# Kernel tuning notes

Hardware: AMD Instinct MI355X
Metric: run time of the kernel (lower is better)

Reference implementation:

```python
import jax, jax.numpy as jnp
import numpy as np

HEADS = 16
DIM_HEAD = 64


def setup_inputs() -> dict:
    key = jax.random.key(0)
    k1, k2, k3, k4 = jax.random.split(key, 4)
    b, sq, skv, dim = 2, 2048, 2048, 1024
    inner = HEADS * DIM_HEAD
    return {
        "x_q": jax.random.normal(k1, (b, sq, dim), dtype=jnp.float32),
        "x_kv": jax.random.normal(k2, (b, skv, dim), dtype=jnp.float32),
        "W_qkv": jax.random.normal(k3, (dim, 3 * inner), dtype=jnp.float32) * (dim ** -0.5),
        "W_out": jax.random.normal(k4, (inner, dim), dtype=jnp.float32) * (inner ** -0.5),
        "b_out": jnp.zeros((dim,), dtype=jnp.float32),
    }


def reference(x_q, x_kv, W_qkv, W_out, b_out):
    b, sq, dim = x_q.shape
    skv = x_kv.shape[1]
    inner = HEADS * DIM_HEAD
    scale = DIM_HEAD ** -0.5
    # to_qkv on concat([x_q, x_kv], seq) as in the original (bias-free linear)
    qkv = jnp.concatenate([x_q, x_kv], axis=1) @ W_qkv  # [b, sq+skv, 3*inner]
    q, k, v = jnp.split(qkv, 3, axis=-1)
    q = q[:, :sq].reshape(b, sq, HEADS, DIM_HEAD).transpose(0, 2, 1, 3)   # [b,h,sq,d]
    k = k[:, sq:].reshape(b, skv, HEADS, DIM_HEAD).transpose(0, 2, 1, 3)  # [b,h,skv,d]
    v = v[:, sq:].reshape(b, skv, HEADS, DIM_HEAD).transpose(0, 2, 1, 3)  # [b,h,skv,d]
    dots = jnp.einsum('bhqd,bhkd->bhqk', q, k) * scale
    attn = jax.nn.softmax(dots, axis=-1)  # dropout p=0.0 -> identity
    out = jnp.einsum('bhqk,bhkd->bhqd', attn, v)
    out = out.transpose(0, 2, 1, 3).reshape(b, sq, inner)
    return out @ W_out + b_out
```

## Files before the change

kernel.cpp:

```cpp
#include <hip/hip_runtime.h>


typedef __attribute__((ext_vector_type(8))) short short8;
typedef __attribute__((ext_vector_type(4))) short short4v;
typedef __attribute__((ext_vector_type(4))) float floatx4;

#define QSCALE 0.18033688f

#if __has_builtin(__builtin_amdgcn_exp2f)
#define EXP2(x) __builtin_amdgcn_exp2f(x)
#else
#define EXP2(x) exp2f(x)
#endif

__device__ __forceinline__ ushort f2b(float f) {
  union { float f; unsigned u; } x; x.f = f;
  unsigned r = (x.u + 0x7fffu + ((x.u >> 16) & 1u)) >> 16;
  return (ushort)r;
}

__device__ __forceinline__ unsigned f2b2(float a, float b) {
  union { float f; unsigned u; } x, y; x.f = a; y.f = b;
  return __builtin_amdgcn_perm(y.u + 0x8000u, x.u + 0x8000u, 0x07060302u);
}

#define GLL(gp, lp)                                                            \
  __builtin_amdgcn_global_load_lds(                                            \
      (const __attribute__((address_space(1))) void*)(gp),                     \
      (__attribute__((address_space(3))) void*)(lp), 16, 0, 0)

__global__ void cvt2(const float* __restrict__ a, const float* __restrict__ bsrc,
                     ushort* __restrict__ oa, ushort* __restrict__ ob, int n) {
  int half = gridDim.x >> 1;
  bool lo = (int)blockIdx.x < half;
  const float* in = lo ? a : bsrc;
  ushort* out = lo ? oa : ob;
  int bid = lo ? blockIdx.x : blockIdx.x - half;
  int stride = half * blockDim.x * 4;
  for (int i = (bid * blockDim.x + threadIdx.x) * 4; i < n; i += stride) {
    float4 v = *(const float4*)(in + i);
    uint2 o;
    o.x = f2b2(v.x, v.y);
    o.y = f2b2(v.z, v.w);
    *(uint2*)(out + i) = o;
  }
}

__global__ void transposeW(const float* __restrict__ Wqkv, ushort* __restrict__ WqkvT,
                           const float* __restrict__ Wout, ushort* __restrict__ WoutT) {
  __shared__ float tile[32][33];
  bool first = blockIdx.x < 96;
  const float* in = first ? Wqkv : Wout;
  ushort* out = first ? WqkvT : WoutT;
  int N = first ? 3072 : 1024;
  int bx = first ? blockIdx.x : blockIdx.x - 96;
  int k0 = blockIdx.y * 32, n0 = bx * 32;
  int tx = threadIdx.x, ty = threadIdx.y;
#pragma unroll
  for (int i = 0; i < 32; i += 8)
    tile[ty + i][tx] = in[(size_t)(k0 + ty + i) * N + n0 + tx];
  __syncthreads();
#pragma unroll
  for (int i = 0; i < 32; i += 8)
    out[(size_t)(n0 + ty + i) * 1024 + k0 + tx] = f2b(tile[tx][ty + i]);
}

__global__ __launch_bounds__(256, 3) void gemm_qkv(
    const ushort* __restrict__ Aq, const ushort* __restrict__ Akv,
    const ushort* __restrict__ Bt,
    ushort* __restrict__ Cq, ushort* __restrict__ Ck, ushort* __restrict__ Cv) {
  __shared__ __align__(16) ushort As[2][128 * 32];
  __shared__ __align__(16) ushort Bs[2][128 * 32];
  const int n0 = blockIdx.x * 128, m0 = blockIdx.y * 128;
  const ushort* A = (blockIdx.x >= 8) ? Akv : Aq;
  const int t = threadIdx.x;
  const int w = t >> 6, lane = t & 63, dl = lane & 15, g = lane >> 4;
  const int wm = (w >> 1) * 64, wn = (w & 1) * 64;
  const int K = 1024;

  auto stage = [&](int buf, int k0) {
#pragma unroll
    for (int p = 0; p < 2; p++) {
      int j = t + p * 256;
      int row = j >> 2, slot = j & 3, c = (slot - row) & 3;
      GLL(A + (size_t)(m0 + row) * K + k0 + c * 8, &As[buf][j * 8]);
    }
#pragma unroll
    for (int p = 0; p < 2; p++) {
      int j = t + p * 256;
      int row = j >> 2, slot = j & 3, c = (slot - row) & 3;
      GLL(Bt + (size_t)(n0 + row) * K + k0 + c * 8, &Bs[buf][j * 8]);
    }
  };

  const floatx4 fz = {0.f, 0.f, 0.f, 0.f};
  floatx4 acc[4][4];
#pragma unroll
  for (int i = 0; i < 4; i++)
#pragma unroll
    for (int j = 0; j < 4; j++) acc[i][j] = fz;

  stage(0, 0);
  for (int kt = 0; kt < 32; kt++) {
    int cur = kt & 1;
    __builtin_amdgcn_s_waitcnt(0);
    __syncthreads();
    if (kt + 1 < 32) stage(cur ^ 1, (kt + 1) * 32);
    short8 af[4], bf[4];
#pragma unroll
    for (int mt = 0; mt < 4; mt++) {
      int row = wm + mt * 16 + dl;
      af[mt] = *(const short8*)&As[cur][row * 32 + ((g + row) & 3) * 8];
    }
#pragma unroll
    for (int nt = 0; nt < 4; nt++) {
      int row = wn + nt * 16 + dl;
      bf[nt] = *(const short8*)&Bs[cur][row * 32 + ((g + row) & 3) * 8];
    }
#pragma unroll
    for (int mt = 0; mt < 4; mt++)
#pragma unroll
      for (int nt = 0; nt < 4; nt++)
        acc[mt][nt] = __builtin_amdgcn_mfma_f32_16x16x32_bf16(af[mt], bf[nt], acc[mt][nt], 0, 0, 0);
  }

#pragma unroll
  for (int mt = 0; mt < 4; mt++)
#pragma unroll
    for (int nt = 0; nt < 4; nt++) {
      int gcol = n0 + wn + nt * 16 + dl;
      int row0 = m0 + wm + mt * 16 + g * 4;
      if (gcol < 1024) {
#pragma unroll
        for (int r = 0; r < 4; r++)
          Cq[(size_t)(row0 + r) * 1024 + gcol] = f2b(acc[mt][nt][r] * QSCALE);
      } else if (gcol < 2048) {
#pragma unroll
        for (int r = 0; r < 4; r++)
          Ck[(size_t)(row0 + r) * 1024 + gcol - 1024] = f2b(acc[mt][nt][r]);
      } else {
        uint2 pk;
        pk.x = f2b2(acc[mt][nt][0], acc[mt][nt][1]);
        pk.y = f2b2(acc[mt][nt][2], acc[mt][nt][3]);
        *(uint2*)(Cv + ((size_t)(row0 >> 11) * 1024 + (gcol - 2048)) * 2048 +
                  (row0 & 2047)) = pk;
      }
    }
}

__global__ __launch_bounds__(256, 3) void gemm_out(
    const ushort* __restrict__ A, const ushort* __restrict__ Bt,
    float* __restrict__ C, const float* __restrict__ bias) {
  __shared__ __align__(16) ushort As[2][128 * 64];
  __shared__ __align__(16) ushort Bs[2][64 * 64];
  const int n0 = blockIdx.x * 64, m0 = blockIdx.y * 128;
  const int t = threadIdx.x;
  const int w = t >> 6, lane = t & 63, dl = lane & 15, g = lane >> 4;
  const int wm = (w >> 1) * 64, wn = (w & 1) * 32;
  const int K = 1024;

  auto stage = [&](int buf, int k0) {
#pragma unroll
    for (int p = 0; p < 4; p++) {
      int j = t + p * 256;
      int row = j >> 3, slot = j & 7, c = (slot - row) & 7;
      GLL(A + (size_t)(m0 + row) * K + k0 + c * 8, &As[buf][j * 8]);
    }
#pragma unroll
    for (int p = 0; p < 2; p++) {
      int j = t + p * 256;
      int row = j >> 3, slot = j & 7, c = (slot - row) & 7;
      GLL(Bt + (size_t)(n0 + row) * K + k0 + c * 8, &Bs[buf][j * 8]);
    }
  };

  const floatx4 fz = {0.f, 0.f, 0.f, 0.f};
  floatx4 acc[4][2];
#pragma unroll
  for (int i = 0; i < 4; i++)
#pragma unroll
    for (int j = 0; j < 2; j++) acc[i][j] = fz;

  stage(0, 0);
  for (int kt = 0; kt < 16; kt++) {
    int cur = kt & 1;
    __builtin_amdgcn_s_waitcnt(0);
    __syncthreads();
    if (kt + 1 < 16) stage(cur ^ 1, (kt + 1) * 64);
#pragma unroll
    for (int ks = 0; ks < 2; ks++) {
      short8 af[4], bf[2];
#pragma unroll
      for (int mt = 0; mt < 4; mt++) {
        int row = wm + mt * 16 + dl;
        af[mt] = *(const short8*)&As[cur][row * 64 + ((ks * 4 + g + row) & 7) * 8];
      }
#pragma unroll
      for (int nt = 0; nt < 2; nt++) {
        int row = wn + nt * 16 + dl;
        bf[nt] = *(const short8*)&Bs[cur][row * 64 + ((ks * 4 + g + row) & 7) * 8];
      }
#pragma unroll
      for (int mt = 0; mt < 4; mt++)
#pragma unroll
        for (int nt = 0; nt < 2; nt++)
          acc[mt][nt] = __builtin_amdgcn_mfma_f32_16x16x32_bf16(af[mt], bf[nt], acc[mt][nt], 0, 0, 0);
    }
  }
#pragma unroll
  for (int mt = 0; mt < 4; mt++)
#pragma unroll
    for (int nt = 0; nt < 2; nt++) {
      int gcol = n0 + wn + nt * 16 + dl;
      int row0 = m0 + wm + mt * 16 + g * 4;
      float badd = bias[gcol];
#pragma unroll
      for (int r = 0; r < 4; r++)
        C[(size_t)(row0 + r) * 1024 + gcol] = acc[mt][nt][r] + badd;
    }
}

__global__ __launch_bounds__(256, 2) void attn(
    const ushort* __restrict__ Qb,
    const ushort* __restrict__ Kb,
    const ushort* __restrict__ Vt,
    ushort* __restrict__ Ob) {
  __shared__ __align__(16) ushort Ks[2][64 * 64];
  __shared__ __align__(16) ushort Vs[2][64 * 64];
  __shared__ __align__(16) ushort Pq[128 * 64];

  const int bh = blockIdx.x, b = bh >> 4, h = bh & 15;
  const int q0 = blockIdx.y * 128;
  const int t = threadIdx.x, w = t >> 6, lane = t & 63, dl = lane & 15, g = lane >> 4;

  const ushort* Kg = Kb + (size_t)(b * 2048) * 1024 + h * 64;
  const ushort* Vg = Vt + (size_t)(b * 1024 + h * 64) * 2048;

  short8 bq[2][2];
#pragma unroll
  for (int nt = 0; nt < 2; nt++) {
    int qa = q0 + w * 32 + nt * 16 + dl;
    const ushort* qrow = Qb + (size_t)(b * 2048 + qa) * 1024 + h * 64;
    bq[nt][0] = *(const short8*)(qrow + g * 8);
    bq[nt][1] = *(const short8*)(qrow + 32 + g * 8);
  }

  auto stageK = [&](int buf, int kv0) {
#pragma unroll
    for (int p = 0; p < 2; p++) {
      int j = t + p * 256;
      int row = j >> 3, slot = j & 7, c = (slot - row) & 7;
      GLL(Kg + (size_t)(kv0 + row) * 1024 + c * 8, &Ks[buf][j * 8]);
    }
  };
  auto stageV = [&](int buf, int kv0) {
#pragma unroll
    for (int p = 0; p < 2; p++) {
      int j = t + p * 256;
      int row = j >> 3, slot = j & 7, c = (slot - row) & 7;
      GLL(Vg + (size_t)row * 2048 + kv0 + c * 8, &Vs[buf][j * 8]);
    }
  };
  stageK(0, 0);
  stageV(0, 0);

  const floatx4 fz = {0.f, 0.f, 0.f, 0.f};
  floatx4 o[4][2];
#pragma unroll
  for (int i = 0; i < 4; i++)
#pragma unroll
    for (int n = 0; n < 2; n++) o[i][n] = fz;
  floatx4 l4[2] = {fz, fz};

  for (int it = 0; it < 32; it++) {
    int cur = it & 1;
    __builtin_amdgcn_s_waitcnt(0);
    __syncthreads();
    if (it + 1 < 32) { stageK(cur ^ 1, (it + 1) * 64); stageV(cur ^ 1, (it + 1) * 64); }

    floatx4 s[4][2];
#pragma unroll
    for (int mt = 0; mt < 4; mt++)
#pragma unroll
      for (int nt = 0; nt < 2; nt++) s[mt][nt] = fz;
#pragma unroll
    for (int ks = 0; ks < 2; ks++) {
      short8 a[4];
#pragma unroll
      for (int mt = 0; mt < 4; mt++) {
        int row = mt * 16 + dl;
        a[mt] = *(const short8*)&Ks[cur][row * 64 + ((ks * 4 + g + row) & 7) * 8];
      }
#pragma unroll
      for (int mt = 0; mt < 4; mt++)
#pragma unroll
        for (int nt = 0; nt < 2; nt++)
          s[mt][nt] = __builtin_amdgcn_mfma_f32_16x16x32_bf16(a[mt], bq[nt][ks], s[mt][nt], 0, 0, 0);
    }

#pragma unroll
    for (int nt = 0; nt < 2; nt++)
#pragma unroll
      for (int mt = 0; mt < 4; mt++) {
#pragma unroll
        for (int r = 0; r < 4; r++) s[mt][nt][r] = EXP2(s[mt][nt][r]);
        l4[nt] += s[mt][nt];
      }

#pragma unroll
    for (int nt = 0; nt < 2; nt++) {
      int qr = w * 32 + nt * 16 + dl;
#pragma unroll
      for (int mt = 0; mt < 4; mt++) {
        uint2 pk;
        pk.x = f2b2(s[mt][nt][0], s[mt][nt][1]);
        pk.y = f2b2(s[mt][nt][2], s[mt][nt][3]);
        *(uint2*)&Pq[qr * 64 + ((mt * 4 + g + qr) & 15) * 4] = pk;
      }
    }
    asm volatile("" ::: "memory");

#pragma unroll
    for (int ks2 = 0; ks2 < 2; ks2++) {
      short8 av[4], bp[2];
#pragma unroll
      for (int mtd = 0; mtd < 4; mtd++) {
        int row = mtd * 16 + dl;
        av[mtd] = *(const short8*)&Vs[cur][row * 64 + ((ks2 * 4 + g + row) & 7) * 8];
      }
#pragma unroll
      for (int nt = 0; nt < 2; nt++) {
        int qr = w * 32 + nt * 16 + dl;
        int sq = ks2 * 8 + 2 * g;
        short4v lo = *(const short4v*)&Pq[qr * 64 + ((sq + qr) & 15) * 4];
        short4v hi = *(const short4v*)&Pq[qr * 64 + ((sq + 1 + qr) & 15) * 4];
        bp[nt] = short8{lo.x, lo.y, lo.z, lo.w, hi.x, hi.y, hi.z, hi.w};
      }
#pragma unroll
      for (int mtd = 0; mtd < 4; mtd++)
#pragma unroll
        for (int nt = 0; nt < 2; nt++)
          o[mtd][nt] = __builtin_amdgcn_mfma_f32_16x16x32_bf16(av[mtd], bp[nt], o[mtd][nt], 0, 0, 0);
    }
    asm volatile("" ::: "memory");
  }

  float inv_l[2];
#pragma unroll
  for (int nt = 0; nt < 2; nt++) {
    float l = (l4[nt][0] + l4[nt][1]) + (l4[nt][2] + l4[nt][3]);
    l += __shfl_xor(l, 16);
    l += __shfl_xor(l, 32);
    inv_l[nt] = 1.f / l;
  }

#pragma unroll
  for (int nt = 0; nt < 2; nt++) {
    int qr = w * 32 + nt * 16 + dl;
#pragma unroll
    for (int mtd = 0; mtd < 4; mtd++) {
      uint2 pk;
      pk.x = f2b2(o[mtd][nt][0] * inv_l[nt], o[mtd][nt][1] * inv_l[nt]);
      pk.y = f2b2(o[mtd][nt][2] * inv_l[nt], o[mtd][nt][3] * inv_l[nt]);
      *(uint2*)&Pq[qr * 64 + ((mtd * 4 + g + qr) & 15) * 4] = pk;
    }
  }
  asm volatile("" ::: "memory");
#pragma unroll
  for (int p = 0; p < 4; p++) {
    int j = lane + p * 64;
    int r32 = j >> 3, c = j & 7;
    int qr = w * 32 + r32;
    short4v lo = *(const short4v*)&Pq[qr * 64 + ((2 * c + qr) & 15) * 4];
    short4v hi = *(const short4v*)&Pq[qr * 64 + ((2 * c + 1 + qr) & 15) * 4];
    short8 v = {lo.x, lo.y, lo.z, lo.w, hi.x, hi.y, hi.z, hi.w};
    *(short8*)(Ob + (size_t)(b * 2048 + q0 + qr) * 1024 + h * 64 + c * 8) = v;
  }
}

extern "C" void kernel_launch(void* const* d_in, const int* in_sizes, int n_in,
                              void* d_out, int out_size, void* d_ws, size_t ws_size,
                              hipStream_t stream) {
  const float* x_q  = (const float*)d_in[0];
  const float* x_kv = (const float*)d_in[1];
  const float* Wqkv = (const float*)d_in[2];
  const float* Wout = (const float*)d_in[3];
  const float* bout = (const float*)d_in[4];
  float* out = (float*)d_out;

  char* p = (char*)d_ws;
  ushort* Xq    = (ushort*)p; p += (size_t)4096 * 1024 * 2;
  ushort* Xkv   = (ushort*)p; p += (size_t)4096 * 1024 * 2;
  ushort* WqkvT = (ushort*)p; p += (size_t)3072 * 1024 * 2;
  ushort* WoutT = (ushort*)p; p += (size_t)1024 * 1024 * 2;
  ushort* Qb    = (ushort*)p; p += (size_t)4096 * 1024 * 2;
  ushort* Kb    = (ushort*)p; p += (size_t)4096 * 1024 * 2;
  ushort* Vt    = (ushort*)p; p += (size_t)2 * 1024 * 2048 * 2;
  ushort* Ob    = (ushort*)p; p += (size_t)4096 * 1024 * 2;

  cvt2<<<2048, 256, 0, stream>>>(x_q, x_kv, Xq, Xkv, 4096 * 1024);
  transposeW<<<dim3(128, 32), dim3(32, 8), 0, stream>>>(Wqkv, WqkvT, Wout, WoutT);
  gemm_qkv<<<dim3(24, 32), 256, 0, stream>>>(Xq, Xkv, WqkvT, Qb, Kb, Vt);
  attn<<<dim3(32, 16), 256, 0, stream>>>(Qb, Kb, Vt, Ob);
  gemm_out<<<dim3(16, 32), 256, 0, stream>>>(Ob, WoutT, out, bout);
}
```

Baseline: 197.9 us.

## Split attention KV tile across wave pairs and halve query tile per block

The attention kernel now processes 64 queries per block instead of 128. Its four waves form two query groups times two KV halves, each wave covering 32 KV columns per tile. Partial outputs and row sums from the two KV halves are reduced through shared memory at the end, and the grid doubles to 1024 blocks with launch bounds raised to 4 blocks per SM. The aim is more parallelism and occupancy, at the cost of re-streaming K/V per block (twice the global K/V traffic), an extra LDS reduction, and more register pressure under the tighter launch bound.

```diff
diff --git a/kernel.cpp b/kernel.cpp
--- a/kernel.cpp
+++ b/kernel.cpp
@@ -220,18 +220,19 @@
     }
 }
 
-__global__ __launch_bounds__(256, 2) void attn(
+__global__ __launch_bounds__(256, 4) void attn(
     const ushort* __restrict__ Qb,
     const ushort* __restrict__ Kb,
     const ushort* __restrict__ Vt,
     ushort* __restrict__ Ob) {
   __shared__ __align__(16) ushort Ks[2][64 * 64];
   __shared__ __align__(16) ushort Vs[2][64 * 64];
-  __shared__ __align__(16) ushort Pq[128 * 64];
+  __shared__ __align__(16) ushort Pq[64 * 64];
 
   const int bh = blockIdx.x, b = bh >> 4, h = bh & 15;
-  const int q0 = blockIdx.y * 128;
+  const int q0 = blockIdx.y * 64;
   const int t = threadIdx.x, w = t >> 6, lane = t & 63, dl = lane & 15, g = lane >> 4;
+  const int wq = w & 1, wkv = w >> 1;
 
   const ushort* Kg = Kb + (size_t)(b * 2048) * 1024 + h * 64;
   const ushort* Vg = Vt + (size_t)(b * 1024 + h * 64) * 2048;
@@ -239,7 +240,7 @@
   short8 bq[2][2];
 #pragma unroll
   for (int nt = 0; nt < 2; nt++) {
-    int qa = q0 + w * 32 + nt * 16 + dl;
+    int qa = q0 + wq * 32 + nt * 16 + dl;
     const ushort* qrow = Qb + (size_t)(b * 2048 + qa) * 1024 + h * 64;
     bq[nt][0] = *(const short8*)(qrow + g * 8);
     bq[nt][1] = *(const short8*)(qrow + 32 + g * 8);
@@ -278,21 +279,21 @@
     __syncthreads();
     if (it + 1 < 32) { stageK(cur ^ 1, (it + 1) * 64); stageV(cur ^ 1, (it + 1) * 64); }
 
-    floatx4 s[4][2];
-#pragma unroll
-    for (int mt = 0; mt < 4; mt++)
+    floatx4 s[2][2];
+#pragma unroll
+    for (int mt = 0; mt < 2; mt++)
 #pragma unroll
       for (int nt = 0; nt < 2; nt++) s[mt][nt] = fz;
 #pragma unroll
     for (int ks = 0; ks < 2; ks++) {
-      short8 a[4];
-#pragma unroll
-      for (int mt = 0; mt < 4; mt++) {
-        int row = mt * 16 + dl;
+      short8 a[2];
+#pragma unroll
+      for (int mt = 0; mt < 2; mt++) {
+        int row = wkv * 32 + mt * 16 + dl;
         a[mt] = *(const short8*)&Ks[cur][row * 64 + ((ks * 4 + g + row) & 7) * 8];
       }
 #pragma unroll
-      for (int mt = 0; mt < 4; mt++)
+      for (int mt = 0; mt < 2; mt++)
 #pragma unroll
         for (int nt = 0; nt < 2; nt++)
           s[mt][nt] = __builtin_amdgcn_mfma_f32_16x16x32_bf16(a[mt], bq[nt][ks], s[mt][nt], 0, 0, 0);
@@ -301,7 +302,7 @@
 #pragma unroll
     for (int nt = 0; nt < 2; nt++)
 #pragma unroll
-      for (int mt = 0; mt < 4; mt++) {
+      for (int mt = 0; mt < 2; mt++) {
 #pragma unroll
         for (int r = 0; r < 4; r++) s[mt][nt][r] = EXP2(s[mt][nt][r]);
         l4[nt] += s[mt][nt];
@@ -309,72 +310,95 @@
 
 #pragma unroll
     for (int nt = 0; nt < 2; nt++) {
-      int qr = w * 32 + nt * 16 + dl;
-#pragma unroll
-      for (int mt = 0; mt < 4; mt++) {
+      int qr = wq * 32 + nt * 16 + dl;
+#pragma unroll
+      for (int mt = 0; mt < 2; mt++) {
+        int kvq = wkv * 8 + mt * 4 + g;
         uint2 pk;
         pk.x = f2b2(s[mt][nt][0], s[mt][nt][1]);
         pk.y = f2b2(s[mt][nt][2], s[mt][nt][3]);
-        *(uint2*)&Pq[qr * 64 + ((mt * 4 + g + qr) & 15) * 4] = pk;
+        *(uint2*)&Pq[qr * 64 + ((kvq + qr) & 15) * 4] = pk;
       }
     }
     asm volatile("" ::: "memory");
 
-#pragma unroll
-    for (int ks2 = 0; ks2 < 2; ks2++) {
-      short8 av[4], bp[2];
-#pragma unroll
-      for (int mtd = 0; mtd < 4; mtd++) {
-        int row = mtd * 16 + dl;
-        av[mtd] = *(const short8*)&Vs[cur][row * 64 + ((ks2 * 4 + g + row) & 7) * 8];
-      }
-#pragma unroll
-      for (int nt = 0; nt < 2; nt++) {
-        int qr = w * 32 + nt * 16 + dl;
-        int sq = ks2 * 8 + 2 * g;
-        short4v lo = *(const short4v*)&Pq[qr * 64 + ((sq + qr) & 15) * 4];
-        short4v hi = *(const short4v*)&Pq[qr * 64 + ((sq + 1 + qr) & 15) * 4];
-        bp[nt] = short8{lo.x, lo.y, lo.z, lo.w, hi.x, hi.y, hi.z, hi.w};
-      }
-#pragma unroll
-      for (int mtd = 0; mtd < 4; mtd++)
-#pragma unroll
-        for (int nt = 0; nt < 2; nt++)
-          o[mtd][nt] = __builtin_amdgcn_mfma_f32_16x16x32_bf16(av[mtd], bp[nt], o[mtd][nt], 0, 0, 0);
-    }
+    short8 av[4], bp[2];
+#pragma unroll
+    for (int mtd = 0; mtd < 4; mtd++) {
+      int row = mtd * 16 + dl;
+      av[mtd] = *(const short8*)&Vs[cur][row * 64 + ((wkv * 4 + g + row) & 7) * 8];
+    }
+#pragma unroll
+    for (int nt = 0; nt < 2; nt++) {
+      int qr = wq * 32 + nt * 16 + dl;
+      int kvq = wkv * 8 + g * 2;
+      short4v lo = *(const short4v*)&Pq[qr * 64 + ((kvq + qr) & 15) * 4];
+      short4v hi = *(const short4v*)&Pq[qr * 64 + ((kvq + 1 + qr) & 15) * 4];
+      bp[nt] = short8{lo.x, lo.y, lo.z, lo.w, hi.x, hi.y, hi.z, hi.w};
+    }
+#pragma unroll
+    for (int mtd = 0; mtd < 4; mtd++)
+#pragma unroll
+      for (int nt = 0; nt < 2; nt++)
+        o[mtd][nt] = __builtin_amdgcn_mfma_f32_16x16x32_bf16(av[mtd], bp[nt], o[mtd][nt], 0, 0, 0);
     asm volatile("" ::: "memory");
   }
 
-  float inv_l[2];
+  float lsum[2];
 #pragma unroll
   for (int nt = 0; nt < 2; nt++) {
     float l = (l4[nt][0] + l4[nt][1]) + (l4[nt][2] + l4[nt][3]);
     l += __shfl_xor(l, 16);
     l += __shfl_xor(l, 32);
-    inv_l[nt] = 1.f / l;
-  }
-
-#pragma unroll
-  for (int nt = 0; nt < 2; nt++) {
-    int qr = w * 32 + nt * 16 + dl;
-#pragma unroll
-    for (int mtd = 0; mtd < 4; mtd++) {
-      uint2 pk;
-      pk.x = f2b2(o[mtd][nt][0] * inv_l[nt], o[mtd][nt][1] * inv_l[nt]);
-      pk.y = f2b2(o[mtd][nt][2] * inv_l[nt], o[mtd][nt][3] * inv_l[nt]);
-      *(uint2*)&Pq[qr * 64 + ((mtd * 4 + g + qr) & 15) * 4] = pk;
-    }
-  }
-  asm volatile("" ::: "memory");
-#pragma unroll
-  for (int p = 0; p < 4; p++) {
-    int j = lane + p * 64;
-    int r32 = j >> 3, c = j & 7;
-    int qr = w * 32 + r32;
-    short4v lo = *(const short4v*)&Pq[qr * 64 + ((2 * c + qr) & 15) * 4];
-    short4v hi = *(const short4v*)&Pq[qr * 64 + ((2 * c + 1 + qr) & 15) * 4];
+    lsum[nt] = l;
+  }
+
+  __syncthreads();
+  float* redO = (float*)Ks;
+  float* redL = (float*)Vs;
+  if (wkv == 1) {
+#pragma unroll
+    for (int mtd = 0; mtd < 4; mtd++)
+#pragma unroll
+      for (int nt = 0; nt < 2; nt++)
+        *(floatx4*)&redO[wq * 2048 + lane * 32 + (mtd * 2 + nt) * 4] = o[mtd][nt];
+#pragma unroll
+    for (int nt = 0; nt < 2; nt++)
+      redL[wq * 32 + nt * 16 + dl] = lsum[nt];
+  }
+  __syncthreads();
+  if (wkv == 0) {
+    float inv_l[2];
+#pragma unroll
+    for (int nt = 0; nt < 2; nt++)
+      inv_l[nt] = 1.f / (lsum[nt] + redL[wq * 32 + nt * 16 + dl]);
+#pragma unroll
+    for (int mtd = 0; mtd < 4; mtd++)
+#pragma unroll
+      for (int nt = 0; nt < 2; nt++)
+        o[mtd][nt] += *(const floatx4*)&redO[wq * 2048 + lane * 32 + (mtd * 2 + nt) * 4];
+#pragma unroll
+    for (int nt = 0; nt < 2; nt++) {
+      int qr = wq * 32 + nt * 16 + dl;
+#pragma unroll
+      for (int mtd = 0; mtd < 4; mtd++) {
+        int dq = mtd * 4 + g;
+        uint2 pk;
+        pk.x = f2b2(o[mtd][nt][0] * inv_l[nt], o[mtd][nt][1] * inv_l[nt]);
+        pk.y = f2b2(o[mtd][nt][2] * inv_l[nt], o[mtd][nt][3] * inv_l[nt]);
+        *(uint2*)&Pq[qr * 64 + ((dq + qr) & 15) * 4] = pk;
+      }
+    }
+  }
+  __syncthreads();
+#pragma unroll
+  for (int p = 0; p < 2; p++) {
+    int j = t + p * 256;
+    int row = j >> 3, c = j & 7;
+    short4v lo = *(const short4v*)&Pq[row * 64 + ((2 * c + row) & 15) * 4];
+    short4v hi = *(const short4v*)&Pq[row * 64 + ((2 * c + 1 + row) & 15) * 4];
     short8 v = {lo.x, lo.y, lo.z, lo.w, hi.x, hi.y, hi.z, hi.w};
-    *(short8*)(Ob + (size_t)(b * 2048 + q0 + qr) * 1024 + h * 64 + c * 8) = v;
+    *(short8*)(Ob + (size_t)(b * 2048 + q0 + row) * 1024 + h * 64 + c * 8) = v;
   }
 }
 
@@ -401,6 +425,6 @@
   cvt2<<<2048, 256, 0, stream>>>(x_q, x_kv, Xq, Xkv, 4096 * 1024);
   transposeW<<<dim3(128, 32), dim3(32, 8), 0, stream>>>(Wqkv, WqkvT, Wout, WoutT);
   gemm_qkv<<<dim3(24, 32), 256, 0, stream>>>(Xq, Xkv, WqkvT, Qb, Kb, Vt);
-  attn<<<dim3(32, 16), 256, 0, stream>>>(Qb, Kb, Vt, Ob);
+  attn<<<dim3(32, 32), 256, 0, stream>>>(Qb, Kb, Vt, Ob);
   gemm_out<<<dim3(16, 32), 256, 0, stream>>>(Ob, WoutT, out, bout);
 }
```

Result: slower. 203.4 us (+2.8%).

## Merge prep kernels and stage V-transpose epilogue through LDS for coalesced stores

Applied to the files above, without the earlier changes.

Merges the input conversion and weight-transpose kernels into one launch to remove a kernel launch and the gap between them. In the QKV GEMM, the V-tile epilogue now writes the transposed tile into shared memory (padded stride 136) and then emits 16-byte coalesced stores to the transposed V buffer, replacing scattered 8-byte stores. The shared buffer grows slightly to hold the transposed tile, which may affect occupancy. The epilogue also adds extra barriers.

```diff
diff --git a/kernel.cpp b/kernel.cpp
--- a/kernel.cpp
+++ b/kernel.cpp
@@ -29,33 +29,37 @@
       (const __attribute__((address_space(1))) void*)(gp),                     \
       (__attribute__((address_space(3))) void*)(lp), 16, 0, 0)
 
-__global__ void cvt2(const float* __restrict__ a, const float* __restrict__ bsrc,
-                     ushort* __restrict__ oa, ushort* __restrict__ ob, int n) {
-  int half = gridDim.x >> 1;
-  bool lo = (int)blockIdx.x < half;
-  const float* in = lo ? a : bsrc;
-  ushort* out = lo ? oa : ob;
-  int bid = lo ? blockIdx.x : blockIdx.x - half;
-  int stride = half * blockDim.x * 4;
-  for (int i = (bid * blockDim.x + threadIdx.x) * 4; i < n; i += stride) {
-    float4 v = *(const float4*)(in + i);
-    uint2 o;
-    o.x = f2b2(v.x, v.y);
-    o.y = f2b2(v.z, v.w);
-    *(uint2*)(out + i) = o;
-  }
-}
-
-__global__ void transposeW(const float* __restrict__ Wqkv, ushort* __restrict__ WqkvT,
-                           const float* __restrict__ Wout, ushort* __restrict__ WoutT) {
+__global__ void prep(const float* __restrict__ xq, const float* __restrict__ xkv,
+                     ushort* __restrict__ oq, ushort* __restrict__ okv,
+                     const float* __restrict__ Wqkv, ushort* __restrict__ WqkvT,
+                     const float* __restrict__ Wout, ushort* __restrict__ WoutT) {
   __shared__ float tile[32][33];
-  bool first = blockIdx.x < 96;
+  int bid = blockIdx.x;
+  const int n = 4096 * 1024;
+  if (bid < 2048) {
+    bool lo = bid < 1024;
+    const float* in = lo ? xq : xkv;
+    ushort* out = lo ? oq : okv;
+    int b2 = lo ? bid : bid - 1024;
+    int stride = 1024 * 256 * 4;
+    for (int i = (b2 * 256 + (int)threadIdx.x) * 4; i < n; i += stride) {
+      float4 v = *(const float4*)(in + i);
+      uint2 o;
+      o.x = f2b2(v.x, v.y);
+      o.y = f2b2(v.z, v.w);
+      *(uint2*)(out + i) = o;
+    }
+    return;
+  }
+  int tb = bid - 2048;
+  int bx = tb & 127, by = tb >> 7;
+  bool first = bx < 96;
   const float* in = first ? Wqkv : Wout;
   ushort* out = first ? WqkvT : WoutT;
   int N = first ? 3072 : 1024;
-  int bx = first ? blockIdx.x : blockIdx.x - 96;
-  int k0 = blockIdx.y * 32, n0 = bx * 32;
-  int tx = threadIdx.x, ty = threadIdx.y;
+  int bxx = first ? bx : bx - 96;
+  int k0 = by * 32, n0 = bxx * 32;
+  int tx = threadIdx.x & 31, ty = threadIdx.x >> 5;
 #pragma unroll
   for (int i = 0; i < 32; i += 8)
     tile[ty + i][tx] = in[(size_t)(k0 + ty + i) * N + n0 + tx];
@@ -69,8 +73,9 @@
     const ushort* __restrict__ Aq, const ushort* __restrict__ Akv,
     const ushort* __restrict__ Bt,
     ushort* __restrict__ Cq, ushort* __restrict__ Ck, ushort* __restrict__ Cv) {
-  __shared__ __align__(16) ushort As[2][128 * 32];
-  __shared__ __align__(16) ushort Bs[2][128 * 32];
+  __shared__ __align__(16) ushort smem[17408];
+  ushort* Asb = smem;
+  ushort* Bsb = smem + 8192;
   const int n0 = blockIdx.x * 128, m0 = blockIdx.y * 128;
   const ushort* A = (blockIdx.x >= 8) ? Akv : Aq;
   const int t = threadIdx.x;
@@ -83,13 +88,13 @@
     for (int p = 0; p < 2; p++) {
       int j = t + p * 256;
       int row = j >> 2, slot = j & 3, c = (slot - row) & 3;
-      GLL(A + (size_t)(m0 + row) * K + k0 + c * 8, &As[buf][j * 8]);
+      GLL(A + (size_t)(m0 + row) * K + k0 + c * 8, &Asb[buf * 4096 + j * 8]);
     }
 #pragma unroll
     for (int p = 0; p < 2; p++) {
       int j = t + p * 256;
       int row = j >> 2, slot = j & 3, c = (slot - row) & 3;
-      GLL(Bt + (size_t)(n0 + row) * K + k0 + c * 8, &Bs[buf][j * 8]);
+      GLL(Bt + (size_t)(n0 + row) * K + k0 + c * 8, &Bsb[buf * 4096 + j * 8]);
     }
   };
 
@@ -110,12 +115,12 @@
 #pragma unroll
     for (int mt = 0; mt < 4; mt++) {
       int row = wm + mt * 16 + dl;
-      af[mt] = *(const short8*)&As[cur][row * 32 + ((g + row) & 3) * 8];
+      af[mt] = *(const short8*)&Asb[cur * 4096 + row * 32 + ((g + row) & 3) * 8];
     }
 #pragma unroll
     for (int nt = 0; nt < 4; nt++) {
       int row = wn + nt * 16 + dl;
-      bf[nt] = *(const short8*)&Bs[cur][row * 32 + ((g + row) & 3) * 8];
+      bf[nt] = *(const short8*)&Bsb[cur * 4096 + row * 32 + ((g + row) & 3) * 8];
     }
 #pragma unroll
     for (int mt = 0; mt < 4; mt++)
@@ -124,28 +129,48 @@
         acc[mt][nt] = __builtin_amdgcn_mfma_f32_16x16x32_bf16(af[mt], bf[nt], acc[mt][nt], 0, 0, 0);
   }
 
-#pragma unroll
-  for (int mt = 0; mt < 4; mt++)
-#pragma unroll
-    for (int nt = 0; nt < 4; nt++) {
-      int gcol = n0 + wn + nt * 16 + dl;
-      int row0 = m0 + wm + mt * 16 + g * 4;
-      if (gcol < 1024) {
-#pragma unroll
-        for (int r = 0; r < 4; r++)
-          Cq[(size_t)(row0 + r) * 1024 + gcol] = f2b(acc[mt][nt][r] * QSCALE);
-      } else if (gcol < 2048) {
-#pragma unroll
-        for (int r = 0; r < 4; r++)
-          Ck[(size_t)(row0 + r) * 1024 + gcol - 1024] = f2b(acc[mt][nt][r]);
-      } else {
+  if (blockIdx.x < 16) {
+#pragma unroll
+    for (int mt = 0; mt < 4; mt++)
+#pragma unroll
+      for (int nt = 0; nt < 4; nt++) {
+        int gcol = n0 + wn + nt * 16 + dl;
+        int row0 = m0 + wm + mt * 16 + g * 4;
+        if (gcol < 1024) {
+#pragma unroll
+          for (int r = 0; r < 4; r++)
+            Cq[(size_t)(row0 + r) * 1024 + gcol] = f2b(acc[mt][nt][r] * QSCALE);
+        } else {
+#pragma unroll
+          for (int r = 0; r < 4; r++)
+            Ck[(size_t)(row0 + r) * 1024 + gcol - 1024] = f2b(acc[mt][nt][r]);
+        }
+      }
+  } else {
+    __syncthreads();
+#pragma unroll
+    for (int mt = 0; mt < 4; mt++)
+#pragma unroll
+      for (int nt = 0; nt < 4; nt++) {
+        int ncol = wn + nt * 16 + dl;
+        int mrow = wm + mt * 16 + g * 4;
         uint2 pk;
         pk.x = f2b2(acc[mt][nt][0], acc[mt][nt][1]);
         pk.y = f2b2(acc[mt][nt][2], acc[mt][nt][3]);
-        *(uint2*)(Cv + ((size_t)(row0 >> 11) * 1024 + (gcol - 2048)) * 2048 +
-                  (row0 & 2047)) = pk;
-      }
-    }
+        *(uint2*)&smem[ncol * 136 + mrow] = pk;
+      }
+    __syncthreads();
+    int hd0 = n0 - 2048;
+    int bb = m0 >> 11;
+    int kv0 = m0 & 2047;
+#pragma unroll
+    for (int p = 0; p < 8; p++) {
+      int j = t + p * 256;
+      int row = j >> 4, c = j & 15;
+      short8 v = *(const short8*)&smem[row * 136 + c * 8];
+      *(short8*)(Cv + ((size_t)(bb * 1024 + hd0 + row)) * 2048 + kv0 + c * 8) = v;
+    }
+  }
 }
 
 __global__ __launch_bounds__(256, 3) void gemm_out(
@@ -398,8 +423,7 @@
   ushort* Vt    = (ushort*)p; p += (size_t)2 * 1024 * 2048 * 2;
   ushort* Ob    = (ushort*)p; p += (size_t)4096 * 1024 * 2;
 
-  cvt2<<<2048, 256, 0, stream>>>(x_q, x_kv, Xq, Xkv, 4096 * 1024);
-  transposeW<<<dim3(128, 32), dim3(32, 8), 0, stream>>>(Wqkv, WqkvT, Wout, WoutT);
+  prep<<<6144, 256, 0, stream>>>(x_q, x_kv, Xq, Xkv, Wqkv, WqkvT, Wout, WoutT);
   gemm_qkv<<<dim3(24, 32), 256, 0, stream>>>(Xq, Xkv, WqkvT, Qb, Kb, Vt);
   attn<<<dim3(32, 16), 256, 0, stream>>>(Qb, Kb, Vt, Ob);
   gemm_out<<<dim3(16, 32), 256, 0, stream>>>(Ob, WoutT, out, bout);
```

After: 196.9 us. About the same (-0.5%).
